# Kernel optimization log

Hardware: AMD Instinct MI355X
Metric: run time of the kernel (lower is better)

Reference implementation:

```python
import jax, jax.numpy as jnp
import numpy as np

W = 128
POS_FREQ = 10  # -> 3*10*2 = 60 encoded dims
VIEW_FREQ = 4  # -> 3*4*2 = 24 encoded dims


def freq_encode(v, n_freq):
    # tcnn 'Frequency' encoding: sin/cos of 2^j * pi * x per input dim.
    scales = (2.0 ** jnp.arange(n_freq, dtype=v.dtype)) * jnp.pi  # [F]
    ang = v[..., :, None] * scales  # [N, 3, F]
    enc = jnp.stack([jnp.sin(ang), jnp.cos(ang)], axis=-1)  # [N, 3, F, 2]
    return enc.reshape(v.shape[0], -1)  # [N, 3*F*2]


def mlp(h, weights):
    # tcnn FullyFusedMLP: bias-free, ReLU on hidden layers, linear output.
    for Wm in weights[:-1]:
        h = jax.nn.relu(h @ Wm)
    return h @ weights[-1]


def setup_inputs():
    key = jax.random.key(0)
    ks = jax.random.split(key, 10)
    N = 1048576

    def w(k, fan_in, fan_out):
        s = (1.0 / np.sqrt(fan_in)).astype(np.float32)
        return jax.random.uniform(k, (fan_in, fan_out), jnp.float32, -s, s)

    return {
        "x": jax.random.uniform(ks[0], (N, 6), jnp.float32),
        "Wd1_0": w(ks[1], 60, W),
        "Wd1_1": w(ks[2], W, W),
        "Wd1_2": w(ks[3], W, W),
        "Wd2_0": w(ks[4], 60 + W, W),
        "Wd2_1": w(ks[5], W, W),
        "Wd2_2": w(ks[6], W, W),
        "Wd2_3": w(ks[7], W, W + 1),
        "Wc_0": w(ks[8], 24 + W, W),
        "Wc_1": w(ks[9], W, 3),
    }


def reference(x, Wd1_0, Wd1_1, Wd1_2, Wd2_0, Wd2_1, Wd2_2, Wd2_3, Wc_0, Wc_1):
    pos, view = x[:, :3], x[:, 3:6]
    # Density MLP
    enc_pos = freq_encode(pos, POS_FREQ)                # [N, 60]
    part1 = mlp(enc_pos, [Wd1_0, Wd1_1, Wd1_2])          # [N, 128]
    dens_out = mlp(jnp.concatenate([enc_pos, part1], -1),
                   [Wd2_0, Wd2_1, Wd2_2, Wd2_3])         # [N, 129]
    blending = jax.nn.sigmoid(dens_out[:, :1])           # [N, 1]
    feature = dens_out[:, 1:]                            # [N, 128]
    density = feature[:, 0:1]                            # [N, 1]
    # Color MLP
    enc_view = freq_encode(view, VIEW_FREQ)              # [N, 24]
    rgb = mlp(jnp.concatenate([enc_view, feature], -1), [Wc_0, Wc_1])  # [N, 3]
    return jnp.concatenate([rgb, density, blending], -1)  # [N, 5]
```

## Files before the change

kernel.cpp:

```cpp
#include <hip/hip_runtime.h>
#include <cstdint>
#include <cstddef>

typedef __attribute__((ext_vector_type(8))) __bf16 bf16x8;
typedef __attribute__((ext_vector_type(16))) float floatx16;

struct SrcPtrs { const float* p[9]; };


__global__ void prep_zero(unsigned short* __restrict__ ws) {
  uint4* p = (uint4*)ws;
  const int n = 147456 / 8;
  for (int i = blockIdx.x * blockDim.x + threadIdx.x; i < n; i += gridDim.x * blockDim.x)
    p[i] = make_uint4(0u, 0u, 0u, 0u);
}

__global__ void prep_fill(SrcPtrs sp, unsigned short* __restrict__ ws) {
  const int m  = blockIdx.x >> 4;
  const int sl = blockIdx.x & 15;
  const int K[9]  = {60, 128, 128, 188, 128, 128, 128, 152, 128};
  const int N[9]  = {128, 128, 128, 128, 128, 128, 129, 128, 3};
  const int TT[9] = {64, 128, 128, 192, 128, 128, 128, 192, 128};
  const unsigned OFF[9] = {0u, 8192u, 24576u, 40960u, 65536u, 81920u, 98304u, 118784u, 143360u};
  const int Km = K[m], Nm = N[m], Tm = TT[m];
  const float* __restrict__ src = sp.p[m];
  unsigned short* __restrict__ dst = ws + OFF[m];
  const int tot = Km * Nm;
  for (int i = sl * 256 + (int)threadIdx.x; i < tot; i += 16 * 256) {
    int k = i / Nm;
    int n = i - k * Nm;
    int kk = k, row = n;
    if (m == 3) kk = (k < 60) ? 128 + k : k - 60;
    if (m == 7) kk = (k < 24) ? 128 + k : k - 24;
    if (m == 6) row = (n == 0) ? 128 : n - 1;
    int c = (kk >> 3) ^ (row & 7);
    int phys = (c << 3) | (kk & 7);
    dst[row * Tm + phys] = __builtin_bit_cast(unsigned short, (__bf16)src[i]);
  }
}


__device__ __forceinline__ unsigned pk2(float a, float b) {
  unsigned short ua = __builtin_bit_cast(unsigned short, (__bf16)a);
  unsigned short ub = __builtin_bit_cast(unsigned short, (__bf16)b);
  return (unsigned)ua | ((unsigned)ub << 16);
}

__device__ __forceinline__ void stage16(const void* g, void* l) {
  __builtin_amdgcn_global_load_lds(
      (const __attribute__((address_space(1))) unsigned int*)g,
      (__attribute__((address_space(3))) unsigned int*)l, 16, 0, 0);
}

template <int KIND>
__device__ __forceinline__ bf16x8 trig_frag(const float (&x)[6], int q2, int sl) {
  bf16x8 r;
#pragma unroll
  for (int j = 0; j < 8; ++j) {
    const int kA = 16 * sl + j;
    const int kB = 16 * sl + 8 + j;
    int dA, dB; float scA, scB; bool vA, vB;
    if (KIND == 0) {
      vA = kA < 60; vB = kB < 60;
      dA = kA / 20; dB = kB / 20;
      scA = (float)(1 << ((kA % 20) >> 1)) * 0.5f;
      scB = (float)(1 << ((kB % 20) >> 1)) * 0.5f;
    } else {
      vA = kA < 24; vB = kB < 24;
      dA = 3 + (kA >> 3); dB = 3 + (kB >> 3);
      scA = (float)(1 << ((kA & 7) >> 1)) * 0.5f;
      scB = (float)(1 << ((kB & 7) >> 1)) * 0.5f;
    }
    float v  = q2 ? x[dB] : x[dA];
    float sc = q2 ? scB : scA;
    bool ok  = q2 ? vB : vA;
    float rev = v * sc;
    float t = (j & 1) ? __builtin_amdgcn_cosf(rev) : __builtin_amdgcn_sinf(rev);
    r[j] = (__bf16)(ok ? t : 0.0f);
  }
  return r;
}

template <int T, int SL, int ST, int KIND, int NT, bool RELU, int OUTM, int ROWS>
__device__ __forceinline__ void run_layer(const unsigned short* __restrict__ wsrc,
                                          unsigned short* __restrict__ sWt,
                                          uint2 (&pkv)[2][16],
                                          const float (&x0)[6], const float (&x1)[6],
                                          float* __restrict__ out, int base, int tid) {
  const int lane = tid & 63;
  const int w = tid >> 6;
  const int q2 = lane >> 5;
  const int l31 = lane & 31;
  constexpr int S = SL + ST;

  __syncthreads();

  {
    const uint4* __restrict__ src = (const uint4*)wsrc;
    uint4* __restrict__ dst = (uint4*)sWt;
    constexpr int NI = (ROWS * T / 8) / 256;
#pragma unroll
    for (int i = 0; i < NI; ++i)
      stage16(src + i * 256 + tid, dst + ((i * 256 + tid) & ~63));
  }

  bf16x8 bf[2][S > 0 ? S : 1];
#pragma unroll
  for (int s = 0; s < SL; ++s) {
#pragma unroll
    for (int m = 0; m < 2; ++m) {
      uint2 p0 = pkv[m][2 * s], p1 = pkv[m][2 * s + 1];
      unsigned sh0x = __shfl_xor(p0.x, 32, 64);
      unsigned sh0y = __shfl_xor(p0.y, 32, 64);
      unsigned sh1x = __shfl_xor(p1.x, 32, 64);
      unsigned sh1y = __shfl_xor(p1.y, 32, 64);
      uint4 u = make_uint4(q2 ? sh1x : p0.x, q2 ? sh1y : p0.y,
                           q2 ? p1.x : sh0x, q2 ? p1.y : sh0y);
      bf[m][s] = __builtin_bit_cast(bf16x8, u);
    }
  }
#pragma unroll
  for (int j = 0; j < ST; ++j) {
    bf[0][SL + j] = trig_frag<KIND>(x0, q2, j);
    bf[1][SL + j] = trig_frag<KIND>(x1, q2, j);
  }

  __syncthreads();

  const int pt0 = base + w * 64 + l31;
  const int pt1 = pt0 + 32;
#pragma unroll
  for (int t = 0; t < NT; ++t) {
    floatx16 a0, a1;
#pragma unroll
    for (int i = 0; i < 16; ++i) { a0[i] = 0.0f; a1[i] = 0.0f; }
#pragma unroll
    for (int s = 0; s < S; ++s) {
      bf16x8 A = *(const bf16x8*)&sWt[(t * 32 + l31) * T + (((2 * s + q2) ^ (l31 & 7)) << 3)];
      a0 = __builtin_amdgcn_mfma_f32_32x32x16_bf16(A, bf[0][s], a0, 0, 0, 0);
      a1 = __builtin_amdgcn_mfma_f32_32x32x16_bf16(A, bf[1][s], a1, 0, 0, 0);
    }
    if (OUTM == 2) {
      if (q2 == 0) {
        float* o0 = out + (size_t)pt0 * 5;
        o0[0] = a0[0]; o0[1] = a0[1]; o0[2] = a0[2];
        float* o1 = out + (size_t)pt1 * 5;
        o1[0] = a1[0]; o1[1] = a1[1]; o1[2] = a1[2];
      }
    } else {
      if (OUTM == 0 || t < 4) {
#pragma unroll
        for (int gg = 0; gg < 4; ++gg) {
          float b0 = a0[4 * gg], b1 = a0[4 * gg + 1], b2 = a0[4 * gg + 2], b3 = a0[4 * gg + 3];
          float c0 = a1[4 * gg], c1 = a1[4 * gg + 1], c2 = a1[4 * gg + 2], c3 = a1[4 * gg + 3];
          if (RELU) {
            b0 = fmaxf(b0, 0.f); b1 = fmaxf(b1, 0.f); b2 = fmaxf(b2, 0.f); b3 = fmaxf(b3, 0.f);
            c0 = fmaxf(c0, 0.f); c1 = fmaxf(c1, 0.f); c2 = fmaxf(c2, 0.f); c3 = fmaxf(c3, 0.f);
          }
          pkv[0][4 * t + gg] = make_uint2(pk2(b0, b1), pk2(b2, b3));
          pkv[1][4 * t + gg] = make_uint2(pk2(c0, c1), pk2(c2, c3));
        }
      }
      if (OUTM == 1 && q2 == 0) {
        if (t == 0) {
          out[(size_t)pt0 * 5 + 3] = a0[0];
          out[(size_t)pt1 * 5 + 3] = a1[0];
        }
        if (t == 4) {
          out[(size_t)pt0 * 5 + 4] = 1.0f / (1.0f + __expf(-a0[0]));
          out[(size_t)pt1 * 5 + 4] = 1.0f / (1.0f + __expf(-a1[0]));
        }
      }
    }
  }
}

__global__ __launch_bounds__(256, 2) void nerf_main(const float* __restrict__ x,
                                                    const unsigned short* __restrict__ ws,
                                                    float* __restrict__ out) {
  __shared__ __align__(16) unsigned short sWt[24576];

  const int tid = (int)threadIdx.x;
  const int base = (int)blockIdx.x * 256;
  const int w = tid >> 6;
  const int l31 = tid & 31;
  const int pt0 = base + w * 64 + l31;

  float x0[6], x1[6];
  {
    const float* a = x + (size_t)pt0 * 6;
    const float* b = x + (size_t)(pt0 + 32) * 6;
#pragma unroll
    for (int c = 0; c < 3; ++c) {
      float2 u = *(const float2*)(a + 2 * c);
      float2 v = *(const float2*)(b + 2 * c);
      x0[2 * c] = u.x; x0[2 * c + 1] = u.y;
      x1[2 * c] = v.x; x1[2 * c + 1] = v.y;
    }
  }

  uint2 pkv[2][16];
#pragma unroll
  for (int m = 0; m < 2; ++m)
#pragma unroll
    for (int j = 0; j < 16; ++j) pkv[m][j] = make_uint2(0u, 0u);

  run_layer< 64, 0, 4, 0, 4, true , 0, 128>(ws + 0u,      sWt, pkv, x0, x1, out, base, tid);
  run_layer<128, 8, 0, 0, 4, true , 0, 128>(ws + 8192u,   sWt, pkv, x0, x1, out, base, tid);
  run_layer<128, 8, 0, 0, 4, false, 0, 128>(ws + 24576u,  sWt, pkv, x0, x1, out, base, tid);
  run_layer<192, 8, 4, 0, 4, true , 0, 128>(ws + 40960u,  sWt, pkv, x0, x1, out, base, tid);
  run_layer<128, 8, 0, 0, 4, true , 0, 128>(ws + 65536u,  sWt, pkv, x0, x1, out, base, tid);
  run_layer<128, 8, 0, 0, 4, true , 0, 128>(ws + 81920u,  sWt, pkv, x0, x1, out, base, tid);
  run_layer<128, 8, 0, 0, 5, false, 1, 160>(ws + 98304u,  sWt, pkv, x0, x1, out, base, tid);
  run_layer<192, 8, 2, 1, 4, true , 0, 128>(ws + 118784u, sWt, pkv, x0, x1, out, base, tid);
  run_layer<128, 8, 0, 0, 1, false, 2,  32>(ws + 143360u, sWt, pkv, x0, x1, out, base, tid);
}

extern "C" void kernel_launch(void* const* d_in, const int* in_sizes, int n_in,
                              void* d_out, int out_size, void* d_ws, size_t ws_size,
                              hipStream_t stream) {
  (void)n_in; (void)out_size; (void)ws_size;
  const float* x = (const float*)d_in[0];
  SrcPtrs sp;
  for (int i = 0; i < 9; ++i) sp.p[i] = (const float*)d_in[1 + i];
  unsigned short* ws = (unsigned short*)d_ws;
  float* out = (float*)d_out;
  const int N = in_sizes[0] / 6;

  prep_zero<<<72, 256, 0, stream>>>(ws);
  prep_fill<<<144, 256, 0, stream>>>(sp, ws);
  nerf_main<<<N / 256, 256, 0, stream>>>(x, ws, out);
}
```

Baseline: 394.0 us.

## Double-buffer weight chunks in LDS and prefetch next chunk during MFMA

```diff
diff --git a/kernel.cpp b/kernel.cpp
--- a/kernel.cpp
+++ b/kernel.cpp
@@ -40,6 +40,15 @@
 }
 
 
+#if defined(__has_builtin)
+#if __has_builtin(__builtin_amdgcn_permlane32_swap)
+#define HAVE_PLSWAP 1
+#endif
+#endif
+#ifndef HAVE_PLSWAP
+#define HAVE_PLSWAP 0
+#endif
+
 __device__ __forceinline__ unsigned pk2(float a, float b) {
   unsigned short ua = __builtin_bit_cast(unsigned short, (__bf16)a);
   unsigned short ub = __builtin_bit_cast(unsigned short, (__bf16)b);
@@ -50,6 +59,19 @@
   __builtin_amdgcn_global_load_lds(
       (const __attribute__((address_space(1))) unsigned int*)g,
       (__attribute__((address_space(3))) unsigned int*)l, 16, 0, 0);
+}
+
+__device__ __forceinline__ void half_swap(unsigned a, unsigned b, int q2,
+                                          unsigned& lo, unsigned& hi) {
+#if HAVE_PLSWAP
+  auto r = __builtin_amdgcn_permlane32_swap(a, b, false, false);
+  lo = r[0]; hi = r[1];
+#else
+  unsigned sa = __shfl_xor(a, 32, 64);
+  unsigned sb = __shfl_xor(b, 32, 64);
+  lo = q2 ? sb : a;
+  hi = q2 ? b : sa;
+#endif
 }
 
 template <int KIND>
@@ -81,94 +103,114 @@
   return r;
 }
 
-template <int T, int SL, int ST, int KIND, int NT, bool RELU, int OUTM, int ROWS>
+template <int T, int SL, int ST, int TSRC, int NT, int CT, int PP0, bool RELU, int OUTM>
 __device__ __forceinline__ void run_layer(const unsigned short* __restrict__ wsrc,
+                                          const unsigned short* __restrict__ nsrc, int nbytes,
                                           unsigned short* __restrict__ sWt,
                                           uint2 (&pkv)[2][16],
+                                          const bf16x8 (&pkt)[2][4],
                                           const float (&x0)[6], const float (&x1)[6],
                                           float* __restrict__ out, int base, int tid) {
   const int lane = tid & 63;
   const int w = tid >> 6;
   const int q2 = lane >> 5;
   const int l31 = lane & 31;
+  const int swz = l31 & 7;
   constexpr int S = SL + ST;
 
-  __syncthreads();
-
-  {
-    const uint4* __restrict__ src = (const uint4*)wsrc;
-    uint4* __restrict__ dst = (uint4*)sWt;
-    constexpr int NI = (ROWS * T / 8) / 256;
-#pragma unroll
-    for (int i = 0; i < NI; ++i)
-      stage16(src + i * 256 + tid, dst + ((i * 256 + tid) & ~63));
-  }
-
-  bf16x8 bf[2][S > 0 ? S : 1];
+  bf16x8 bf[2][S];
 #pragma unroll
   for (int s = 0; s < SL; ++s) {
 #pragma unroll
     for (int m = 0; m < 2; ++m) {
       uint2 p0 = pkv[m][2 * s], p1 = pkv[m][2 * s + 1];
-      unsigned sh0x = __shfl_xor(p0.x, 32, 64);
-      unsigned sh0y = __shfl_xor(p0.y, 32, 64);
-      unsigned sh1x = __shfl_xor(p1.x, 32, 64);
-      unsigned sh1y = __shfl_xor(p1.y, 32, 64);
-      uint4 u = make_uint4(q2 ? sh1x : p0.x, q2 ? sh1y : p0.y,
-                           q2 ? p1.x : sh0x, q2 ? p1.y : sh0y);
+      unsigned w0, w2, w1, w3;
+      half_swap(p0.x, p1.x, q2, w0, w2);
+      half_swap(p0.y, p1.y, q2, w1, w3);
+      uint4 u = make_uint4(w0, w1, w2, w3);
       bf[m][s] = __builtin_bit_cast(bf16x8, u);
     }
   }
 #pragma unroll
   for (int j = 0; j < ST; ++j) {
-    bf[0][SL + j] = trig_frag<KIND>(x0, q2, j);
-    bf[1][SL + j] = trig_frag<KIND>(x1, q2, j);
-  }
-
-  __syncthreads();
+    if (TSRC == 1) {
+      bf[0][SL + j] = pkt[0][j];
+      bf[1][SL + j] = pkt[1][j];
+    } else {
+      bf[0][SL + j] = trig_frag<1>(x0, q2, j);
+      bf[1][SL + j] = trig_frag<1>(x1, q2, j);
+    }
+  }
 
   const int pt0 = base + w * 64 + l31;
   const int pt1 = pt0 + 32;
-#pragma unroll
-  for (int t = 0; t < NT; ++t) {
-    floatx16 a0, a1;
-#pragma unroll
-    for (int i = 0; i < 16; ++i) { a0[i] = 0.0f; a1[i] = 0.0f; }
-#pragma unroll
-    for (int s = 0; s < S; ++s) {
-      bf16x8 A = *(const bf16x8*)&sWt[(t * 32 + l31) * T + (((2 * s + q2) ^ (l31 & 7)) << 3)];
-      a0 = __builtin_amdgcn_mfma_f32_32x32x16_bf16(A, bf[0][s], a0, 0, 0, 0);
-      a1 = __builtin_amdgcn_mfma_f32_32x32x16_bf16(A, bf[1][s], a1, 0, 0, 0);
-    }
-    if (OUTM == 2) {
-      if (q2 == 0) {
-        float* o0 = out + (size_t)pt0 * 5;
-        o0[0] = a0[0]; o0[1] = a0[1]; o0[2] = a0[2];
-        float* o1 = out + (size_t)pt1 * 5;
-        o1[0] = a1[0]; o1[1] = a1[1]; o1[2] = a1[2];
+
+  constexpr int NC = (NT + CT - 1) / CT;
+#pragma unroll
+  for (int c = 0; c < NC; ++c) {
+    const int pp = PP0 ^ (c & 1);
+    __syncthreads();
+    {
+      const unsigned short* src;
+      int bytes;
+      if (c + 1 < NC) {
+        src = wsrc + (c + 1) * CT * 32 * T;
+        bytes = ((NT - (c + 1) * CT) < CT ? (NT - (c + 1) * CT) : CT) * 64 * T;
+      } else {
+        src = nsrc;
+        bytes = nbytes;
       }
-    } else {
-      if (OUTM == 0 || t < 4) {
-#pragma unroll
-        for (int gg = 0; gg < 4; ++gg) {
-          float b0 = a0[4 * gg], b1 = a0[4 * gg + 1], b2 = a0[4 * gg + 2], b3 = a0[4 * gg + 3];
-          float c0 = a1[4 * gg], c1 = a1[4 * gg + 1], c2 = a1[4 * gg + 2], c3 = a1[4 * gg + 3];
-          if (RELU) {
-            b0 = fmaxf(b0, 0.f); b1 = fmaxf(b1, 0.f); b2 = fmaxf(b2, 0.f); b3 = fmaxf(b3, 0.f);
-            c0 = fmaxf(c0, 0.f); c1 = fmaxf(c1, 0.f); c2 = fmaxf(c2, 0.f); c3 = fmaxf(c3, 0.f);
+      const uint4* s4 = (const uint4*)src;
+      uint4* dst = (uint4*)(sWt + (pp ^ 1) * 8192);
+      const int n16 = bytes / 16;
+      for (int i = tid; i < n16; i += 256)
+        stage16(s4 + i, dst + (i & ~63));
+    }
+    const unsigned short* bufp = sWt + pp * 8192;
+#pragma unroll
+    for (int tt = 0; tt < CT; ++tt) {
+      if (c * CT + tt < NT) {
+        const int TILE = c * CT + tt;
+        floatx16 a0, a1;
+#pragma unroll
+        for (int i = 0; i < 16; ++i) { a0[i] = 0.0f; a1[i] = 0.0f; }
+#pragma unroll
+        for (int s = 0; s < S; ++s) {
+          bf16x8 A = *(const bf16x8*)&bufp[(tt * 32 + l31) * T + (((2 * s + q2) ^ swz) << 3)];
+          a0 = __builtin_amdgcn_mfma_f32_32x32x16_bf16(A, bf[0][s], a0, 0, 0, 0);
+          a1 = __builtin_amdgcn_mfma_f32_32x32x16_bf16(A, bf[1][s], a1, 0, 0, 0);
+        }
+        if (OUTM == 2) {
+          if (q2 == 0) {
+            float* o0 = out + (size_t)pt0 * 5;
+            o0[0] = a0[0]; o0[1] = a0[1]; o0[2] = a0[2];
+            float* o1 = out + (size_t)pt1 * 5;
+            o1[0] = a1[0]; o1[1] = a1[1]; o1[2] = a1[2];
           }
-          pkv[0][4 * t + gg] = make_uint2(pk2(b0, b1), pk2(b2, b3));
-          pkv[1][4 * t + gg] = make_uint2(pk2(c0, c1), pk2(c2, c3));
-        }
-      }
-      if (OUTM == 1 && q2 == 0) {
-        if (t == 0) {
-          out[(size_t)pt0 * 5 + 3] = a0[0];
-          out[(size_t)pt1 * 5 + 3] = a1[0];
-        }
-        if (t == 4) {
-          out[(size_t)pt0 * 5 + 4] = 1.0f / (1.0f + __expf(-a0[0]));
-          out[(size_t)pt1 * 5 + 4] = 1.0f / (1.0f + __expf(-a1[0]));
+        } else {
+          if (OUTM == 0 || TILE < 4) {
+#pragma unroll
+            for (int gg = 0; gg < 4; ++gg) {
+              float b0 = a0[4 * gg], b1 = a0[4 * gg + 1], b2 = a0[4 * gg + 2], b3 = a0[4 * gg + 3];
+              float c0 = a1[4 * gg], c1 = a1[4 * gg + 1], c2 = a1[4 * gg + 2], c3 = a1[4 * gg + 3];
+              if (RELU) {
+                b0 = fmaxf(b0, 0.f); b1 = fmaxf(b1, 0.f); b2 = fmaxf(b2, 0.f); b3 = fmaxf(b3, 0.f);
+                c0 = fmaxf(c0, 0.f); c1 = fmaxf(c1, 0.f); c2 = fmaxf(c2, 0.f); c3 = fmaxf(c3, 0.f);
+              }
+              pkv[0][4 * TILE + gg] = make_uint2(pk2(b0, b1), pk2(b2, b3));
+              pkv[1][4 * TILE + gg] = make_uint2(pk2(c0, c1), pk2(c2, c3));
+            }
+          }
+          if (OUTM == 1 && q2 == 0) {
+            if (TILE == 0) {
+              out[(size_t)pt0 * 5 + 3] = a0[0];
+              out[(size_t)pt1 * 5 + 3] = a1[0];
+            }
+            if (TILE == 4) {
+              out[(size_t)pt0 * 5 + 4] = 1.0f / (1.0f + __expf(-a0[0]));
+              out[(size_t)pt1 * 5 + 4] = 1.0f / (1.0f + __expf(-a1[0]));
+            }
+          }
         }
       }
     }
@@ -178,13 +220,23 @@
 __global__ __launch_bounds__(256, 2) void nerf_main(const float* __restrict__ x,
                                                     const unsigned short* __restrict__ ws,
                                                     float* __restrict__ out) {
-  __shared__ __align__(16) unsigned short sWt[24576];
+  __shared__ __align__(16) unsigned short sWt[2 * 8192];
 
   const int tid = (int)threadIdx.x;
   const int base = (int)blockIdx.x * 256;
+  const int lane = tid & 63;
   const int w = tid >> 6;
-  const int l31 = tid & 31;
+  const int q2 = lane >> 5;
+  const int l31 = lane & 31;
   const int pt0 = base + w * 64 + l31;
+
+  {
+    const uint4* s4 = (const uint4*)ws;
+    uint4* dst = (uint4*)sWt;
+#pragma unroll
+    for (int i = 0; i < 4; ++i)
+      stage16(s4 + i * 256 + tid, dst + ((i * 256 + tid) & ~63));
+  }
 
   float x0[6], x1[6];
   {
@@ -199,21 +251,28 @@
     }
   }
 
+  bf16x8 pkt[2][4];
+#pragma unroll
+  for (int sl = 0; sl < 4; ++sl) {
+    pkt[0][sl] = trig_frag<0>(x0, q2, sl);
+    pkt[1][sl] = trig_frag<0>(x1, q2, sl);
+  }
+
   uint2 pkv[2][16];
 #pragma unroll
   for (int m = 0; m < 2; ++m)
 #pragma unroll
     for (int j = 0; j < 16; ++j) pkv[m][j] = make_uint2(0u, 0u);
 
-  run_layer< 64, 0, 4, 0, 4, true , 0, 128>(ws + 0u,      sWt, pkv, x0, x1, out, base, tid);
-  run_layer<128, 8, 0, 0, 4, true , 0, 128>(ws + 8192u,   sWt, pkv, x0, x1, out, base, tid);
-  run_layer<128, 8, 0, 0, 4, false, 0, 128>(ws + 24576u,  sWt, pkv, x0, x1, out, base, tid);
-  run_layer<192, 8, 4, 0, 4, true , 0, 128>(ws + 40960u,  sWt, pkv, x0, x1, out, base, tid);
-  run_layer<128, 8, 0, 0, 4, true , 0, 128>(ws + 65536u,  sWt, pkv, x0, x1, out, base, tid);
-  run_layer<128, 8, 0, 0, 4, true , 0, 128>(ws + 81920u,  sWt, pkv, x0, x1, out, base, tid);
-  run_layer<128, 8, 0, 0, 5, false, 1, 160>(ws + 98304u,  sWt, pkv, x0, x1, out, base, tid);
-  run_layer<192, 8, 2, 1, 4, true , 0, 128>(ws + 118784u, sWt, pkv, x0, x1, out, base, tid);
-  run_layer<128, 8, 0, 0, 1, false, 2,  32>(ws + 143360u, sWt, pkv, x0, x1, out, base, tid);
+  run_layer< 64, 0, 4, 1, 4, 4, 0, true , 0>(ws + 0u,      ws + 8192u,   16384, sWt, pkv, pkt, x0, x1, out, base, tid);
+  run_layer<128, 8, 0, 0, 4, 2, 1, true , 0>(ws + 8192u,   ws + 24576u,  16384, sWt, pkv, pkt, x0, x1, out, base, tid);
+  run_layer<128, 8, 0, 0, 4, 2, 1, false, 0>(ws + 24576u,  ws + 40960u,  12288, sWt, pkv, pkt, x0, x1, out, base, tid);
+  run_layer<192, 8, 4, 1, 4, 1, 1, true , 0>(ws + 40960u,  ws + 65536u,  16384, sWt, pkv, pkt, x0, x1, out, base, tid);
+  run_layer<128, 8, 0, 0, 4, 2, 1, true , 0>(ws + 65536u,  ws + 81920u,  16384, sWt, pkv, pkt, x0, x1, out, base, tid);
+  run_layer<128, 8, 0, 0, 4, 2, 1, true , 0>(ws + 81920u,  ws + 98304u,  16384, sWt, pkv, pkt, x0, x1, out, base, tid);
+  run_layer<128, 8, 0, 0, 5, 2, 1, false, 1>(ws + 98304u,  ws + 118784u, 12288, sWt, pkv, pkt, x0, x1, out, base, tid);
+  run_layer<192, 8, 2, 2, 4, 1, 0, true , 0>(ws + 118784u, ws + 143360u,  8192, sWt, pkv, pkt, x0, x1, out, base, tid);
+  run_layer<128, 8, 0, 0, 1, 1, 0, false, 2>(ws + 143360u, (const unsigned short*)nullptr, 0, sWt, pkv, pkt, x0, x1, out, base, tid);
 }
 
 extern "C" void kernel_launch(void* const* d_in, const int* in_sizes, int n_in,
```

Result: faster. 375.0 us (-4.8%).

## Load MFMA weight fragments straight from global memory instead of LDS staging

Applied to the files above, without the earlier changes.

```diff
diff --git a/kernel.cpp b/kernel.cpp
--- a/kernel.cpp
+++ b/kernel.cpp
@@ -10,7 +10,7 @@
 
 __global__ void prep_zero(unsigned short* __restrict__ ws) {
   uint4* p = (uint4*)ws;
-  const int n = 147456 / 8;
+  const int n = 143360 / 8;
   for (int i = blockIdx.x * blockDim.x + threadIdx.x; i < n; i += gridDim.x * blockDim.x)
     p[i] = make_uint4(0u, 0u, 0u, 0u);
 }
@@ -20,9 +20,9 @@
   const int sl = blockIdx.x & 15;
   const int K[9]  = {60, 128, 128, 188, 128, 128, 128, 152, 128};
   const int N[9]  = {128, 128, 128, 128, 128, 128, 129, 128, 3};
-  const int TT[9] = {64, 128, 128, 192, 128, 128, 128, 192, 128};
-  const unsigned OFF[9] = {0u, 8192u, 24576u, 40960u, 65536u, 81920u, 98304u, 118784u, 143360u};
-  const int Km = K[m], Nm = N[m], Tm = TT[m];
+  const int SS[9] = {4, 8, 8, 12, 8, 8, 8, 10, 8};
+  const unsigned OFF[9] = {0u, 8192u, 24576u, 40960u, 65536u, 81920u, 98304u, 118784u, 139264u};
+  const int Km = K[m], Nm = N[m], Sm = SS[m];
   const float* __restrict__ src = sp.p[m];
   unsigned short* __restrict__ dst = ws + OFF[m];
   const int tot = Km * Nm;
@@ -33,12 +33,22 @@
     if (m == 3) kk = (k < 60) ? 128 + k : k - 60;
     if (m == 7) kk = (k < 24) ? 128 + k : k - 24;
     if (m == 6) row = (n == 0) ? 128 : n - 1;
-    int c = (kk >> 3) ^ (row & 7);
-    int phys = (c << 3) | (kk & 7);
-    dst[row * Tm + phys] = __builtin_bit_cast(unsigned short, (__bf16)src[i]);
-  }
-}
-
+    const int t = row >> 5, l31 = row & 31;
+    const int s = kk >> 4, q2 = (kk >> 3) & 1, j = kk & 7;
+    dst[(t * Sm + s) * 512 + (q2 * 32 + l31) * 8 + j] =
+        __builtin_bit_cast(unsigned short, (__bf16)src[i]);
+  }
+}
+
+
+#if defined(__has_builtin)
+#if __has_builtin(__builtin_amdgcn_permlane32_swap)
+#define HAVE_PLSWAP 1
+#endif
+#endif
+#ifndef HAVE_PLSWAP
+#define HAVE_PLSWAP 0
+#endif
 
 __device__ __forceinline__ unsigned pk2(float a, float b) {
   unsigned short ua = __builtin_bit_cast(unsigned short, (__bf16)a);
@@ -46,10 +56,17 @@
   return (unsigned)ua | ((unsigned)ub << 16);
 }
 
-__device__ __forceinline__ void stage16(const void* g, void* l) {
-  __builtin_amdgcn_global_load_lds(
-      (const __attribute__((address_space(1))) unsigned int*)g,
-      (__attribute__((address_space(3))) unsigned int*)l, 16, 0, 0);
+__device__ __forceinline__ void half_swap(unsigned a, unsigned b, int q2,
+                                          unsigned& lo, unsigned& hi) {
+#if HAVE_PLSWAP
+  auto r = __builtin_amdgcn_permlane32_swap(a, b, false, false);
+  lo = r[0]; hi = r[1];
+#else
+  unsigned sa = __shfl_xor(a, 32, 64);
+  unsigned sb = __shfl_xor(b, 32, 64);
+  lo = q2 ? sb : a;
+  hi = q2 ? b : sa;
+#endif
 }
 
 template <int KIND>
@@ -81,94 +98,80 @@
   return r;
 }
 
-template <int T, int SL, int ST, int KIND, int NT, bool RELU, int OUTM, int ROWS>
+template <int S, int SL, int NT, bool RELU, int OUTM>
 __device__ __forceinline__ void run_layer(const unsigned short* __restrict__ wsrc,
-                                          unsigned short* __restrict__ sWt,
                                           uint2 (&pkv)[2][16],
-                                          const float (&x0)[6], const float (&x1)[6],
+                                          const bf16x8 (&tail)[2][4],
                                           float* __restrict__ out, int base, int tid) {
   const int lane = tid & 63;
   const int w = tid >> 6;
   const int q2 = lane >> 5;
   const int l31 = lane & 31;
-  constexpr int S = SL + ST;
-
-  __syncthreads();
-
-  {
-    const uint4* __restrict__ src = (const uint4*)wsrc;
-    uint4* __restrict__ dst = (uint4*)sWt;
-    constexpr int NI = (ROWS * T / 8) / 256;
-#pragma unroll
-    for (int i = 0; i < NI; ++i)
-      stage16(src + i * 256 + tid, dst + ((i * 256 + tid) & ~63));
-  }
-
-  bf16x8 bf[2][S > 0 ? S : 1];
+  const int pt0 = base + w * 64 + l31;
+  const int pt1 = pt0 + 32;
+
+  bf16x8 bf[2][SL > 0 ? SL : 1];
 #pragma unroll
   for (int s = 0; s < SL; ++s) {
 #pragma unroll
     for (int m = 0; m < 2; ++m) {
       uint2 p0 = pkv[m][2 * s], p1 = pkv[m][2 * s + 1];
-      unsigned sh0x = __shfl_xor(p0.x, 32, 64);
-      unsigned sh0y = __shfl_xor(p0.y, 32, 64);
-      unsigned sh1x = __shfl_xor(p1.x, 32, 64);
-      unsigned sh1y = __shfl_xor(p1.y, 32, 64);
-      uint4 u = make_uint4(q2 ? sh1x : p0.x, q2 ? sh1y : p0.y,
-                           q2 ? p1.x : sh0x, q2 ? p1.y : sh0y);
+      unsigned w0, w1, w2, w3;
+      half_swap(p0.x, p1.x, q2, w0, w2);
+      half_swap(p0.y, p1.y, q2, w1, w3);
+      uint4 u = make_uint4(w0, w1, w2, w3);
       bf[m][s] = __builtin_bit_cast(bf16x8, u);
     }
   }
-#pragma unroll
-  for (int j = 0; j < ST; ++j) {
-    bf[0][SL + j] = trig_frag<KIND>(x0, q2, j);
-    bf[1][SL + j] = trig_frag<KIND>(x1, q2, j);
-  }
-
-  __syncthreads();
-
-  const int pt0 = base + w * 64 + l31;
-  const int pt1 = pt0 + 32;
+
+  const uint4* __restrict__ wp = (const uint4*)wsrc;
 #pragma unroll
   for (int t = 0; t < NT; ++t) {
-    floatx16 a0, a1;
-#pragma unroll
-    for (int i = 0; i < 16; ++i) { a0[i] = 0.0f; a1[i] = 0.0f; }
+    floatx16 acc[2];
+#pragma unroll
+    for (int i = 0; i < 16; ++i) { acc[0][i] = 0.0f; acc[1][i] = 0.0f; }
 #pragma unroll
     for (int s = 0; s < S; ++s) {
-      bf16x8 A = *(const bf16x8*)&sWt[(t * 32 + l31) * T + (((2 * s + q2) ^ (l31 & 7)) << 3)];
-      a0 = __builtin_amdgcn_mfma_f32_32x32x16_bf16(A, bf[0][s], a0, 0, 0, 0);
-      a1 = __builtin_amdgcn_mfma_f32_32x32x16_bf16(A, bf[1][s], a1, 0, 0, 0);
+      uint4 a4 = wp[(t * S + s) * 64 + lane];
+      bf16x8 A = __builtin_bit_cast(bf16x8, a4);
+      const int si = (s < SL) ? s : 0;
+      const int ti = (s < SL) ? 0 : (s - SL);
+      bf16x8 B0 = (s < SL) ? bf[0][si] : tail[0][ti];
+      bf16x8 B1 = (s < SL) ? bf[1][si] : tail[1][ti];
+      acc[0] = __builtin_amdgcn_mfma_f32_32x32x16_bf16(A, B0, acc[0], 0, 0, 0);
+      acc[1] = __builtin_amdgcn_mfma_f32_32x32x16_bf16(A, B1, acc[1], 0, 0, 0);
     }
     if (OUTM == 2) {
       if (q2 == 0) {
         float* o0 = out + (size_t)pt0 * 5;
-        o0[0] = a0[0]; o0[1] = a0[1]; o0[2] = a0[2];
+        o0[0] = acc[0][0]; o0[1] = acc[0][1]; o0[2] = acc[0][2];
         float* o1 = out + (size_t)pt1 * 5;
-        o1[0] = a1[0]; o1[1] = a1[1]; o1[2] = a1[2];
+        o1[0] = acc[1][0]; o1[1] = acc[1][1]; o1[2] = acc[1][2];
       }
     } else {
       if (OUTM == 0 || t < 4) {
 #pragma unroll
-        for (int gg = 0; gg < 4; ++gg) {
-          float b0 = a0[4 * gg], b1 = a0[4 * gg + 1], b2 = a0[4 * gg + 2], b3 = a0[4 * gg + 3];
-          float c0 = a1[4 * gg], c1 = a1[4 * gg + 1], c2 = a1[4 * gg + 2], c3 = a1[4 * gg + 3];
-          if (RELU) {
-            b0 = fmaxf(b0, 0.f); b1 = fmaxf(b1, 0.f); b2 = fmaxf(b2, 0.f); b3 = fmaxf(b3, 0.f);
-            c0 = fmaxf(c0, 0.f); c1 = fmaxf(c1, 0.f); c2 = fmaxf(c2, 0.f); c3 = fmaxf(c3, 0.f);
+        for (int m = 0; m < 2; ++m) {
+#pragma unroll
+          for (int gg = 0; gg < 4; ++gg) {
+            float b0 = acc[m][4 * gg], b1 = acc[m][4 * gg + 1];
+            float b2 = acc[m][4 * gg + 2], b3 = acc[m][4 * gg + 3];
+            if (RELU) {
+              b0 = fmaxf(b0, 0.f); b1 = fmaxf(b1, 0.f);
+              b2 = fmaxf(b2, 0.f); b3 = fmaxf(b3, 0.f);
+            }
+            pkv[m][4 * t + gg] = make_uint2(pk2(b0, b1), pk2(b2, b3));
           }
-          pkv[0][4 * t + gg] = make_uint2(pk2(b0, b1), pk2(b2, b3));
-          pkv[1][4 * t + gg] = make_uint2(pk2(c0, c1), pk2(c2, c3));
         }
       }
       if (OUTM == 1 && q2 == 0) {
         if (t == 0) {
-          out[(size_t)pt0 * 5 + 3] = a0[0];
-          out[(size_t)pt1 * 5 + 3] = a1[0];
+          out[(size_t)pt0 * 5 + 3] = acc[0][0];
+          out[(size_t)pt1 * 5 + 3] = acc[1][0];
         }
         if (t == 4) {
-          out[(size_t)pt0 * 5 + 4] = 1.0f / (1.0f + __expf(-a0[0]));
-          out[(size_t)pt1 * 5 + 4] = 1.0f / (1.0f + __expf(-a1[0]));
+          out[(size_t)pt0 * 5 + 4] = 1.0f / (1.0f + __expf(-acc[0][0]));
+          out[(size_t)pt1 * 5 + 4] = 1.0f / (1.0f + __expf(-acc[1][0]));
         }
       }
     }
@@ -178,12 +181,12 @@
 __global__ __launch_bounds__(256, 2) void nerf_main(const float* __restrict__ x,
                                                     const unsigned short* __restrict__ ws,
                                                     float* __restrict__ out) {
-  __shared__ __align__(16) unsigned short sWt[24576];
-
   const int tid = (int)threadIdx.x;
   const int base = (int)blockIdx.x * 256;
+  const int lane = tid & 63;
   const int w = tid >> 6;
-  const int l31 = tid & 31;
+  const int q2 = lane >> 5;
+  const int l31 = lane & 31;
   const int pt0 = base + w * 64 + l31;
 
   float x0[6], x1[6];
@@ -199,21 +202,34 @@
     }
   }
 
+  bf16x8 pkt[2][4];
+#pragma unroll
+  for (int sl = 0; sl < 4; ++sl) {
+    pkt[0][sl] = trig_frag<0>(x0, q2, sl);
+    pkt[1][sl] = trig_frag<0>(x1, q2, sl);
+  }
+
   uint2 pkv[2][16];
-#pragma unroll
-  for (int m = 0; m < 2; ++m)
-#pragma unroll
-    for (int j = 0; j < 16; ++j) pkv[m][j] = make_uint2(0u, 0u);
-
-  run_layer< 64, 0, 4, 0, 4, true , 0, 128>(ws + 0u,      sWt, pkv, x0, x1, out, base, tid);
-  run_layer<128, 8, 0, 0, 4, true , 0, 128>(ws + 8192u,   sWt, pkv, x0, x1, out, base, tid);
-  run_layer<128, 8, 0, 0, 4, false, 0, 128>(ws + 24576u,  sWt, pkv, x0, x1, out, base, tid);
-  run_layer<192, 8, 4, 0, 4, true , 0, 128>(ws + 40960u,  sWt, pkv, x0, x1, out, base, tid);
-  run_layer<128, 8, 0, 0, 4, true , 0, 128>(ws + 65536u,  sWt, pkv, x0, x1, out, base, tid);
-  run_layer<128, 8, 0, 0, 4, true , 0, 128>(ws + 81920u,  sWt, pkv, x0, x1, out, base, tid);
-  run_layer<128, 8, 0, 0, 5, false, 1, 160>(ws + 98304u,  sWt, pkv, x0, x1, out, base, tid);
-  run_layer<192, 8, 2, 1, 4, true , 0, 128>(ws + 118784u, sWt, pkv, x0, x1, out, base, tid);
-  run_layer<128, 8, 0, 0, 1, false, 2,  32>(ws + 143360u, sWt, pkv, x0, x1, out, base, tid);
+
+  run_layer< 4, 0, 4, true , 0>(ws + 0u,      pkv, pkt, out, base, tid);
+  run_layer< 8, 8, 4, true , 0>(ws + 8192u,   pkv, pkt, out, base, tid);
+  run_layer< 8, 8, 4, false, 0>(ws + 24576u,  pkv, pkt, out, base, tid);
+  run_layer<12, 8, 4, true , 0>(ws + 40960u,  pkv, pkt, out, base, tid);
+  run_layer< 8, 8, 4, true , 0>(ws + 65536u,  pkv, pkt, out, base, tid);
+  run_layer< 8, 8, 4, true , 0>(ws + 81920u,  pkv, pkt, out, base, tid);
+  run_layer< 8, 8, 5, false, 1>(ws + 98304u,  pkv, pkt, out, base, tid);
+
+  bf16x8 vw[2][4];
+#pragma unroll
+  for (int sl = 0; sl < 2; ++sl) {
+    vw[0][sl] = trig_frag<1>(x0, q2, sl);
+    vw[1][sl] = trig_frag<1>(x1, q2, sl);
+  }
+  vw[0][2] = vw[0][0]; vw[0][3] = vw[0][0];
+  vw[1][2] = vw[1][0]; vw[1][3] = vw[1][0];
+
+  run_layer<10, 8, 4, true , 0>(ws + 118784u, pkv, vw,  out, base, tid);
+  run_layer< 8, 8, 1, false, 2>(ws + 139264u, pkv, pkt, out, base, tid);
 }
 
 extern "C" void kernel_launch(void* const* d_in, const int* in_sizes, int n_in,
@@ -227,7 +243,7 @@
   float* out = (float*)d_out;
   const int N = in_sizes[0] / 6;
 
-  prep_zero<<<72, 256, 0, stream>>>(ws);
+  prep_zero<<<70, 256, 0, stream>>>(ws);
   prep_fill<<<144, 256, 0, stream>>>(sp, ws);
   nerf_main<<<N / 256, 256, 0, stream>>>(x, ws, out);
 }
```

Measured after the change: 434.4 us. 10.2% more time.
